# Kernel optimization log

Hardware: AMD Instinct MI355X
Metric: run time of the kernel (lower is better)

Reference implementation:

```python
import jax, jax.numpy as jnp
import numpy as np

EPS = 1e-7
B, C, IMG = 1024, 3, 32
NCLASS = 10
N_IN, L_IN, L_OUT = 64, 16, 16   # primary caps: 64 capsules of length 16; digit caps length 16
R_ITER = 3


def squash(c, axis):
    dot = jnp.sum(c * c, axis=axis, keepdims=True)
    return dot / (1.0 + dot) / jnp.sqrt(dot + EPS) * c


def conv2d(x, w, b, stride):
    y = jax.lax.conv_general_dilated(x, w, (stride, stride), 'VALID',
                                     dimension_numbers=('NCHW', 'OIHW', 'NCHW'))
    return y + b[None, :, None, None]


def setup_inputs() -> dict:
    key = jax.random.key(0)
    ks = jax.random.split(key, 16)
    inp = {
        'x': jax.random.uniform(ks[0], (B, C, IMG, IMG), dtype=jnp.float32),
        'y': jax.random.randint(ks[1], (B,), 0, NCLASS, dtype=jnp.int64),
        'conv1_w': 0.05 * jax.random.normal(ks[2], (128, C, 3, 3), jnp.float32),
        'conv1_b': jnp.zeros((128,), jnp.float32),
        'conv2_w': 0.05 * jax.random.normal(ks[3], (256, 128, 5, 5), jnp.float32),
        'conv2_b': jnp.zeros((256,), jnp.float32),
        'conv3_w': 0.05 * jax.random.normal(ks[4], (256, 256, 5, 5), jnp.float32),
        'conv3_b': jnp.zeros((256,), jnp.float32),
        'caps_w': 0.05 * jax.random.normal(ks[5], (N_IN, NCLASS, L_IN, L_OUT), jnp.float32),
        'caps_b': 0.05 * jax.random.normal(ks[6], (NCLASS, L_OUT), jnp.float32),
        'fc1_w': 0.05 * jax.random.normal(ks[7], (512, NCLASS * L_OUT), jnp.float32),
        'fc1_b': jnp.zeros((512,), jnp.float32),
        'fc2_w': 0.05 * jax.random.normal(ks[8], (1024, 512), jnp.float32),
        'fc2_b': jnp.zeros((1024,), jnp.float32),
        'fc3_w': 0.05 * jax.random.normal(ks[9], (IMG * IMG * C, 1024), jnp.float32),
        'fc3_b': jnp.zeros((IMG * IMG * C,), jnp.float32),
    }
    return inp


def reference(x, y, conv1_w, conv1_b, conv2_w, conv2_b, conv3_w, conv3_b,
              caps_w, caps_b, fc1_w, fc1_b, fc2_w, fc2_b, fc3_w, fc3_b):
    # CNN blocks
    h = jax.nn.relu(conv2d(x, conv1_w, conv1_b, 2))   # [B,128,15,15]
    h = jax.nn.relu(conv2d(h, conv2_w, conv2_b, 2))   # [B,256,6,6]
    h = jax.nn.relu(conv2d(h, conv3_w, conv3_b, 1))   # [B,256,2,2]

    # Primary capsules: [B,64,16], squashed along capsule-length axis
    prim = squash(h.reshape(h.shape[0], N_IN, L_IN), axis=-1)

    # u_hat[b,i,o,j] = sum_k W[i,o,k,j] * prim[b,i,k]  -> [B,64,10,16]
    u_hat = jnp.einsum('bik,iokj->bioj', prim, caps_w)
    u_hat_det = jax.lax.stop_gradient(u_hat)

    b_ij = jnp.zeros((h.shape[0], N_IN, NCLASS), dtype=u_hat.dtype)
    v = None
    for r in range(R_ITER):
        c_ij = jax.nn.softmax(b_ij, axis=2)           # over output capsules
        uh = u_hat if r == R_ITER - 1 else u_hat_det
        s = jnp.einsum('bio,bioj->boj', c_ij, uh) + caps_b   # [B,10,16]
        v = squash(s, axis=-1)
        if r < R_ITER - 1:
            agree = jnp.einsum('bioj,boj->bio', u_hat_det, jax.lax.stop_gradient(v))
            b_ij = b_ij + agree

    # capsule lengths: [B,10,1,1]
    v_lengths = jnp.sqrt(jnp.sum(v * v, axis=-1, keepdims=True) + EPS)[..., None]

    # reconstruction (mask by true label one-hot)
    one_hot = jax.nn.one_hot(y, NCLASS, dtype=v.dtype)       # [B,10]
    masked = (v * one_hot[:, :, None]).reshape(v.shape[0], NCLASS * L_OUT)
    h1 = jax.nn.relu(masked @ fc1_w.T + fc1_b)
    h2 = jax.nn.relu(h1 @ fc2_w.T + fc2_b)
    decoded = jax.nn.sigmoid(h2 @ fc3_w.T + fc3_b)           # [B,3072]
    return (v_lengths, decoded)
```

## Files before the change

kernel.cpp:

```cpp
#include <hip/hip_runtime.h>
#include <hip/hip_bf16.h>
#include <math.h>

#define EPSF 1e-7f

typedef __attribute__((ext_vector_type(8))) short bhalf8;
typedef __attribute__((ext_vector_type(4))) float floatx4;

__global__ __launch_bounds__(256) void conv1_kernel(
    const float* __restrict__ x, const float* __restrict__ w,
    const float* __restrict__ bias, __hip_bfloat16* __restrict__ out)
{
  __shared__ float wl[3456];
  __shared__ float bl[128];
  const int b = blockIdx.x;
  const int t = threadIdx.x;
  for (int i = t; i < 3456; i += 256) wl[i] = w[i];
  if (t < 128) bl[t] = bias[t];
  __syncthreads();
  if (t >= 225) return;
  const int py = t / 15, px = t % 15;
  const float* xb = x + b * 3072;
  float win[27];
#pragma unroll
  for (int c = 0; c < 3; ++c)
#pragma unroll
    for (int ky = 0; ky < 3; ++ky)
#pragma unroll
      for (int kx = 0; kx < 3; ++kx)
        win[c*9 + ky*3 + kx] = xb[c*1024 + (py*2 + ky)*32 + (px*2 + kx)];
#pragma unroll 1
  for (int oc0 = 0; oc0 < 128; oc0 += 32) {
    __hip_bfloat16 hv[32];
#pragma unroll
    for (int oc = 0; oc < 32; ++oc) {
      const float* wp = &wl[(oc0 + oc)*27];
      float acc = bl[oc0 + oc];
#pragma unroll
      for (int q = 0; q < 27; ++q) acc = fmaf(win[q], wp[q], acc);
      hv[oc] = __float2bfloat16(fmaxf(acc, 0.f));
    }
    uint4* dst = (uint4*)&out[((size_t)b*225 + t)*128 + oc0];
    const uint4* src = (const uint4*)hv;
#pragma unroll
    for (int q = 0; q < 4; ++q) dst[q] = src[q];
  }
}

__global__ __launch_bounds__(256) void prep_kernel(
    const float* __restrict__ conv2w, const float* __restrict__ conv3w,
    const float* __restrict__ capsw,  const float* __restrict__ fc1w,
    const float* __restrict__ fc2w,   const float* __restrict__ fc3w,
    __hip_bfloat16* __restrict__ wt2, __hip_bfloat16* __restrict__ wt3,
    __hip_bfloat16* __restrict__ cwt, float* __restrict__ fc1wt,
    __hip_bfloat16* __restrict__ wf2, __hip_bfloat16* __restrict__ wf3)
{
  const int t = threadIdx.x;
  int b = blockIdx.x;
  if (b < 12288) {
    int i = b*256 + t;
    wf3[i] = __float2bfloat16(fc3w[i]);
    return;
  }
  b -= 12288;
  if (b < 6400) {
    int i = b*256 + t;
    int s = i >> 14, r = i & 16383;
    int oc = r >> 6, kq = r & 63;
    int k = s*64 + kq;
    int tap = k >> 8, ic = k & 255;
    wt3[i] = __float2bfloat16(conv3w[(oc*256 + ic)*25 + tap]);
    return;
  }
  b -= 6400;
  if (b < 3200) {
    int i = b*256 + t;
    int s = i >> 13, r = i & 8191;
    int oc = r >> 5, kq = r & 31;
    int h = (s >= 50) ? 1 : 0;
    int r2 = s - h*50;
    int tap = r2 >> 1, q = r2 & 1;
    int ic = h*64 + q*32 + kq;
    wt2[i] = __float2bfloat16(conv2w[(oc*128 + ic)*25 + tap]);
    return;
  }
  b -= 3200;
  if (b < 2048) {
    int i = b*256 + t;
    wf2[i] = __float2bfloat16(fc2w[i]);
    return;
  }
  b -= 2048;
  if (b < 640) {
    int i2 = b*256 + t;
    int k = i2 & 15, j = (i2 >> 4) & 15, io = i2 >> 8;
    cwt[i2] = __float2bfloat16(capsw[(io*16 + k)*16 + j]);
    return;
  }
  b -= 640;
  {
    int i = b*256 + t;
    int j = i >> 9, n = i & 511;
    fc1wt[i] = fc1w[n*160 + j];
  }
}

__global__ __launch_bounds__(1024) void conv2_mfma_kernel(
    const __hip_bfloat16* __restrict__ a,
    const __hip_bfloat16* __restrict__ wt,
    const float* __restrict__ bias,
    __hip_bfloat16* __restrict__ out)
{
  __shared__ __align__(16) unsigned short Il[4*225*64];
  const int b0   = blockIdx.x * 4;
  const int t    = threadIdx.x;
  const int lane = t & 63;
  const int w    = t >> 6;
  const int wm   = w >> 3;
  const int wn   = w & 7;
  const int n    = lane & 15;
  const int g    = lane >> 4;

  const char* gB = (const char*)wt + (wn*32 + n)*64 + g*16;
  bhalf8 b00 = *(const bhalf8*)(gB);
  bhalf8 b01 = *(const bhalf8*)(gB + 1024);
  bhalf8 b10 = *(const bhalf8*)(gB + 16384);
  bhalf8 b11 = *(const bhalf8*)(gB + 16384 + 1024);

  int Abase[5], em[5];
#pragma unroll
  for (int mt = 0; mt < 5; ++mt) {
    int tile = wm*5 + mt;
    int m = tile*16 + n;
    if (m >= 144) m = 0;
    int img = m / 36, pos = m - img*36;
    int py = pos / 6, px = pos - py*6;
    int pixb = 30*py + 2*px;
    Abase[mt] = (img*225 + pixb) * 128;
    em[mt] = g + m;
  }

  floatx4 acc[5][2];
#pragma unroll
  for (int mt = 0; mt < 5; ++mt)
#pragma unroll
    for (int nt = 0; nt < 2; ++nt)
      acc[mt][nt] = (floatx4){0.f, 0.f, 0.f, 0.f};

  int s = 0;
#pragma unroll 1
  for (int h = 0; h < 2; ++h) {
    if (h) __syncthreads();
    for (int i = t; i < 7200; i += 1024) {
      int img = i / 1800;
      int r = i - img*1800;
      int p = r >> 3, c = r & 7;
      uint4 v = *(const uint4*)((const char*)a +
                ((size_t)(b0+img)*225 + p)*256 + h*128 + c*16);
      int px15 = p % 15, py15 = p / 15;
      int csw = (c + (px15 >> 1) + 6*(py15 >> 1) + ((img & 1) << 2)) & 7;
      *(uint4*)((char*)Il + (img*225 + p)*128 + csw*16) = v;
    }
    __syncthreads();

    int dpix = 0, kx = 0, ky = 0;
#pragma unroll 1
    for (int tap = 0; tap < 25; ++tap) {
      const int doff = dpix << 7;
      const int dsw  = (kx >> 1) + 6*(ky >> 1);
      int a0[5];
#pragma unroll
      for (int mt = 0; mt < 5; ++mt)
        a0[mt] = Abase[mt] + doff + (((em[mt] + dsw) & 7) << 4);

#pragma unroll
      for (int mt = 0; mt < 4; ++mt) {
        bhalf8 av = *(const bhalf8*)((const char*)Il + a0[mt]);
        acc[mt][0] = __builtin_amdgcn_mfma_f32_16x16x32_bf16(av, b00, acc[mt][0], 0, 0, 0);
        acc[mt][1] = __builtin_amdgcn_mfma_f32_16x16x32_bf16(av, b01, acc[mt][1], 0, 0, 0);
      }
      if (wm == 0) {
        bhalf8 av = *(const bhalf8*)((const char*)Il + a0[4]);
        acc[4][0] = __builtin_amdgcn_mfma_f32_16x16x32_bf16(av, b00, acc[4][0], 0, 0, 0);
        acc[4][1] = __builtin_amdgcn_mfma_f32_16x16x32_bf16(av, b01, acc[4][1], 0, 0, 0);
      }
      {
        const int spre = (s + 2 < 100) ? (s + 2) : 99;
        b00 = *(const bhalf8*)(gB + (size_t)spre*16384);
        b01 = *(const bhalf8*)(gB + (size_t)spre*16384 + 1024);
      }
#pragma unroll
      for (int mt = 0; mt < 4; ++mt) {
        bhalf8 av = *(const bhalf8*)((const char*)Il + (a0[mt] ^ 64));
        acc[mt][0] = __builtin_amdgcn_mfma_f32_16x16x32_bf16(av, b10, acc[mt][0], 0, 0, 0);
        acc[mt][1] = __builtin_amdgcn_mfma_f32_16x16x32_bf16(av, b11, acc[mt][1], 0, 0, 0);
      }
      if (wm == 0) {
        bhalf8 av = *(const bhalf8*)((const char*)Il + (a0[4] ^ 64));
        acc[4][0] = __builtin_amdgcn_mfma_f32_16x16x32_bf16(av, b10, acc[4][0], 0, 0, 0);
        acc[4][1] = __builtin_amdgcn_mfma_f32_16x16x32_bf16(av, b11, acc[4][1], 0, 0, 0);
      }
      {
        const int spre = (s + 3 < 100) ? (s + 3) : 99;
        b10 = *(const bhalf8*)(gB + (size_t)spre*16384);
        b11 = *(const bhalf8*)(gB + (size_t)spre*16384 + 1024);
      }
      s += 2;
      if (kx == 4) { kx = 0; ++ky; dpix += 11; } else { ++kx; ++dpix; }
    }
  }

  const float bv0 = bias[wn*32 + n];
  const float bv1 = bias[wn*32 + 16 + n];
#pragma unroll
  for (int mt = 0; mt < 5; ++mt) {
    if (mt < 4 || wm == 0) {
      int tile = wm*5 + mt;
#pragma unroll
      for (int r = 0; r < 4; ++r) {
        int m = tile*16 + g*4 + r;
        int img = m / 36, pos = m - img*36;
        size_t o = (((size_t)(b0+img)*36 + pos) << 8) + wn*32 + n;
        out[o]      = __float2bfloat16(fmaxf(acc[mt][0][r] + bv0, 0.f));
        out[o + 16] = __float2bfloat16(fmaxf(acc[mt][1][r] + bv1, 0.f));
      }
    }
  }
}

__global__ __launch_bounds__(512) void conv3_mfma_kernel(
    const __hip_bfloat16* __restrict__ a,
    const __hip_bfloat16* __restrict__ wt,
    float* __restrict__ pout)
{
  __shared__ __align__(16) unsigned short Il[16*1448];
  const int b0   = blockIdx.x * 16;
  const int kq   = blockIdx.y;
  const int t    = threadIdx.x;
  const int lane = t & 63;
  const int w    = t >> 6;
  const int n    = lane & 15;
  const int g    = lane >> 4;

  for (int i = t; i < 2304; i += 512) {
    int img = i / 144, r = i - img*144;
    int p = r >> 2, c = r & 3;
    uint4 v = *(const uint4*)((const char*)a +
              ((((size_t)(b0+img)*36 + p) << 9) + kq*64 + c*16));
    *(uint4*)((char*)Il + (img*1448 + p*40 + c*8)*2) = v;
  }

  const char* gB = (const char*)wt + (size_t)(w*32 + n)*128 +
                   (kq & 1)*64 + g*16;
  const int kqs = kq >> 1;
  bhalf8 b00, b01, b10, b11;
  b00 = *(const bhalf8*)(gB + (size_t)(0*4 + kqs)*32768);
  b01 = *(const bhalf8*)(gB + (size_t)(0*4 + kqs)*32768 + 2048);
  b10 = *(const bhalf8*)(gB + (size_t)(1*4 + kqs)*32768);
  b11 = *(const bhalf8*)(gB + (size_t)(1*4 + kqs)*32768 + 2048);

  const int d = n >> 2, pos = n & 3;
  const int pb = (pos >> 1)*6 + (pos & 1);
  int ab[4];
#pragma unroll
  for (int mt = 0; mt < 4; ++mt)
    ab[mt] = ((mt*4 + d)*1448 + pb*40 + g*8) * 2;

  floatx4 acc[4][2];
#pragma unroll
  for (int mt = 0; mt < 4; ++mt)
#pragma unroll
    for (int nt = 0; nt < 2; ++nt)
      acc[mt][nt] = (floatx4){0.f, 0.f, 0.f, 0.f};

  __syncthreads();

  int toff = 0, kx = 0;
#pragma unroll 1
  for (int tap = 0; tap < 24; tap += 2) {
#pragma unroll
    for (int mt = 0; mt < 4; ++mt) {
      bhalf8 av = *(const bhalf8*)((const char*)Il + ab[mt] + toff*80);
      acc[mt][0] = __builtin_amdgcn_mfma_f32_16x16x32_bf16(av, b00, acc[mt][0], 0, 0, 0);
      acc[mt][1] = __builtin_amdgcn_mfma_f32_16x16x32_bf16(av, b01, acc[mt][1], 0, 0, 0);
    }
    b00 = *(const bhalf8*)(gB + (size_t)((tap+2)*4 + kqs)*32768);
    b01 = *(const bhalf8*)(gB + (size_t)((tap+2)*4 + kqs)*32768 + 2048);
    if (++kx == 5) { kx = 0; toff += 2; } else ++toff;
#pragma unroll
    for (int mt = 0; mt < 4; ++mt) {
      bhalf8 av = *(const bhalf8*)((const char*)Il + ab[mt] + toff*80);
      acc[mt][0] = __builtin_amdgcn_mfma_f32_16x16x32_bf16(av, b10, acc[mt][0], 0, 0, 0);
      acc[mt][1] = __builtin_amdgcn_mfma_f32_16x16x32_bf16(av, b11, acc[mt][1], 0, 0, 0);
    }
    {
      const int tpre = (tap + 3 <= 24) ? (tap + 3) : 24;
      b10 = *(const bhalf8*)(gB + (size_t)(tpre*4 + kqs)*32768);
      b11 = *(const bhalf8*)(gB + (size_t)(tpre*4 + kqs)*32768 + 2048);
    }
    if (++kx == 5) { kx = 0; toff += 2; } else ++toff;
  }
#pragma unroll
  for (int mt = 0; mt < 4; ++mt) {
    bhalf8 av = *(const bhalf8*)((const char*)Il + ab[mt] + toff*80);
    acc[mt][0] = __builtin_amdgcn_mfma_f32_16x16x32_bf16(av, b00, acc[mt][0], 0, 0, 0);
    acc[mt][1] = __builtin_amdgcn_mfma_f32_16x16x32_bf16(av, b01, acc[mt][1], 0, 0, 0);
  }

  float* po = pout + (size_t)kq*1048576;
#pragma unroll
  for (int mt = 0; mt < 4; ++mt) {
#pragma unroll
    for (int r = 0; r < 4; ++r) {
      int m = mt*16 + g*4 + r;
      int img = m >> 2, p2 = m & 3;
#pragma unroll
      for (int nt = 0; nt < 2; ++nt)
        po[((size_t)(b0+img)*256 + w*32 + nt*16 + n)*4 + p2] = acc[mt][nt][r];
    }
  }
}

__global__ __launch_bounds__(256) void caps_kernel(
    const float* __restrict__ pout, const __hip_bfloat16* __restrict__ cwt,
    const float* __restrict__ cb, const float* __restrict__ c3b,
    const int* __restrict__ y,
    const float* __restrict__ fc1wt, const float* __restrict__ fc1b,
    float* __restrict__ vlen, __hip_bfloat16* __restrict__ h1f)
{
  __shared__ float prim[1024];
  __shared__ float uh[10240];
  __shared__ float bij[640];
  __shared__ float cij[640];
  __shared__ float vv[160];
  const int b = blockIdx.x, t = threadIdx.x;
  {
    const float* pp = pout + (size_t)b*1024 + t*4;
    float4 s4 = *(const float4*)pp;
#pragma unroll
    for (int q = 1; q < 8; ++q) {
      float4 v = *(const float4*)(pp + (size_t)q*1048576);
      s4.x += v.x; s4.y += v.y; s4.z += v.z; s4.w += v.w;
    }
    const float bv = c3b[t];
    float4 h = make_float4(fmaxf(s4.x + bv, 0.f), fmaxf(s4.y + bv, 0.f),
                           fmaxf(s4.z + bv, 0.f), fmaxf(s4.w + bv, 0.f));
    float dd = h.x*h.x + h.y*h.y + h.z*h.z + h.w*h.w;
    dd += __shfl_xor(dd, 1);
    dd += __shfl_xor(dd, 2);
    float sc = dd / (1.f + dd) / sqrtf(dd + EPSF);
    float4 o4 = make_float4(h.x*sc, h.y*sc, h.z*sc, h.w*sc);
    *(float4*)&prim[t*4] = o4;
  }
  for (int f = t; f < 640; f += 256) bij[f] = 0.f;
  __syncthreads();
  for (int f = t; f < 10240; f += 256) {
    const int i = f / 160;
    const uint4* wv = (const uint4*)(cwt + (size_t)f*16);
    uint4 wa = wv[0], wb = wv[1];
    unsigned uw[8] = {wa.x, wa.y, wa.z, wa.w, wb.x, wb.y, wb.z, wb.w};
    const float* pp = prim + i*16;
    float s = 0.f;
#pragma unroll
    for (int q = 0; q < 8; ++q) {
      float lo = __uint_as_float(uw[q] << 16);
      float hi = __uint_as_float(uw[q] & 0xffff0000u);
      s = fmaf(pp[2*q],   lo, s);
      s = fmaf(pp[2*q+1], hi, s);
    }
    uh[f] = s;
  }
  __syncthreads();
  for (int r = 0; r < 3; ++r) {
    if (t < 64) {
      float e[10];
      float mx = -1e30f;
#pragma unroll
      for (int o = 0; o < 10; ++o) { e[o] = bij[t*10 + o]; mx = fmaxf(mx, e[o]); }
      float sum = 0.f;
#pragma unroll
      for (int o = 0; o < 10; ++o) { e[o] = expf(e[o] - mx); sum += e[o]; }
      float inv = 1.f / sum;
#pragma unroll
      for (int o = 0; o < 10; ++o) cij[t*10 + o] = e[o] * inv;
    }
    __syncthreads();
    if (t < 160) {
      const int o = t >> 4;
      float s = cb[t];
      for (int i = 0; i < 64; ++i) s = fmaf(cij[i*10 + o], uh[i*160 + t], s);
      float dd = s*s;
      dd += __shfl_xor(dd, 1); dd += __shfl_xor(dd, 2);
      dd += __shfl_xor(dd, 4); dd += __shfl_xor(dd, 8);
      float sc = dd / (1.f + dd) / sqrtf(dd + EPSF);
      vv[t] = s * sc;
      if (r == 2 && (t & 15) == 0)
        vlen[b*10 + o] = sqrtf(sc*sc*dd + EPSF);
    }
    __syncthreads();
    if (r < 2) {
      for (int f = t; f < 640; f += 256) {
        int i = f / 10, o = f % 10;
        const float* up = &uh[i*160 + o*16];
        const float* vp = &vv[o*16];
        float a = 0.f;
#pragma unroll
        for (int j = 0; j < 16; ++j) a = fmaf(up[j], vp[j], a);
        bij[f] += a;
      }
      __syncthreads();
    }
  }
  const int yb = y[b];
  const float* vy = &vv[yb*16];
  for (int nn = t; nn < 512; nn += 256) {
    float s = fc1b[nn];
#pragma unroll
    for (int k = 0; k < 16; ++k)
      s = fmaf(vy[k], fc1wt[(yb*16 + k)*512 + nn], s);
    h1f[b*512 + nn] = __float2bfloat16(fmaxf(s, 0.f));
  }
}

template<int ACT, int MT, int NT>
__global__ __launch_bounds__(256) void fc_mfma_kernel(
    const __hip_bfloat16* __restrict__ A,
    const __hip_bfloat16* __restrict__ W,
    const float* __restrict__ bias,
    void* __restrict__ outv, int M, int N, int K)
{
  const int t    = threadIdx.x;
  const int lane = t & 63;
  const int w    = t >> 6;
  const int wr   = w >> 1, wc = w & 1;
  const int n    = lane & 15, g = lane >> 4;
  const int m0   = blockIdx.x * (2*MT*16) + wr*(MT*16);
  const int n0   = blockIdx.y * (2*NT*16) + wc*(NT*16);
  const __hip_bfloat16* Ap = A + (size_t)(m0 + n)*K + g*8;
  const __hip_bfloat16* Wp = W + (size_t)(n0 + n)*K + g*8;
  const int steps = K >> 5;

  bhalf8 aa0[MT], aa1[MT], bb0[NT], bb1[NT];
#pragma unroll
  for (int mt = 0; mt < MT; ++mt) {
    aa0[mt] = *(const bhalf8*)(Ap + (size_t)mt*16*K);
    aa1[mt] = *(const bhalf8*)(Ap + (size_t)mt*16*K + 32);
  }
#pragma unroll
  for (int nt = 0; nt < NT; ++nt) {
    bb0[nt] = *(const bhalf8*)(Wp + (size_t)nt*16*K);
    bb1[nt] = *(const bhalf8*)(Wp + (size_t)nt*16*K + 32);
  }

  floatx4 acc[MT][NT];
#pragma unroll
  for (int mt = 0; mt < MT; ++mt)
#pragma unroll
    for (int nt = 0; nt < NT; ++nt)
      acc[mt][nt] = (floatx4){0.f, 0.f, 0.f, 0.f};

#pragma unroll 1
  for (int s = 0; s < steps; s += 2) {
#pragma unroll
    for (int mt = 0; mt < MT; ++mt)
#pragma unroll
      for (int nt = 0; nt < NT; ++nt)
        acc[mt][nt] = __builtin_amdgcn_mfma_f32_16x16x32_bf16(
            aa0[mt], bb0[nt], acc[mt][nt], 0, 0, 0);
    {
      const int spre = (s + 2 < steps) ? (s + 2) : s;
#pragma unroll
      for (int mt = 0; mt < MT; ++mt)
        aa0[mt] = *(const bhalf8*)(Ap + (size_t)mt*16*K + spre*32);
#pragma unroll
      for (int nt = 0; nt < NT; ++nt)
        bb0[nt] = *(const bhalf8*)(Wp + (size_t)nt*16*K + spre*32);
    }
#pragma unroll
    for (int mt = 0; mt < MT; ++mt)
#pragma unroll
      for (int nt = 0; nt < NT; ++nt)
        acc[mt][nt] = __builtin_amdgcn_mfma_f32_16x16x32_bf16(
            aa1[mt], bb1[nt], acc[mt][nt], 0, 0, 0);
    {
      const int spre = (s + 3 < steps) ? (s + 3) : (s + 1);
#pragma unroll
      for (int mt = 0; mt < MT; ++mt)
        aa1[mt] = *(const bhalf8*)(Ap + (size_t)mt*16*K + spre*32);
#pragma unroll
      for (int nt = 0; nt < NT; ++nt)
        bb1[nt] = *(const bhalf8*)(Wp + (size_t)nt*16*K + spre*32);
    }
  }

#pragma unroll
  for (int mt = 0; mt < MT; ++mt) {
#pragma unroll
    for (int r = 0; r < 4; ++r) {
      const int m = m0 + mt*16 + g*4 + r;
#pragma unroll
      for (int nt = 0; nt < NT; ++nt) {
        const int col = n0 + nt*16 + n;
        float v = acc[mt][nt][r] + bias[col];
        if (ACT == 0) {
          ((__hip_bfloat16*)outv)[(size_t)m*N + col] =
              __float2bfloat16(fmaxf(v, 0.f));
        } else {
          ((float*)outv)[(size_t)m*N + col] = 1.f / (1.f + expf(-v));
        }
      }
    }
  }
}

extern "C" void kernel_launch(void* const* d_in, const int* in_sizes, int n_in,
                              void* d_out, int out_size, void* d_ws, size_t ws_size,
                              hipStream_t stream) {
  const float* x       = (const float*)d_in[0];
  const int*   y       = (const int*)  d_in[1];
  const float* conv1_w = (const float*)d_in[2];
  const float* conv1_b = (const float*)d_in[3];
  const float* conv2_w = (const float*)d_in[4];
  const float* conv2_b = (const float*)d_in[5];
  const float* conv3_w = (const float*)d_in[6];
  const float* conv3_b = (const float*)d_in[7];
  const float* caps_w  = (const float*)d_in[8];
  const float* caps_b  = (const float*)d_in[9];
  const float* fc1_w   = (const float*)d_in[10];
  const float* fc1_b   = (const float*)d_in[11];
  const float* fc2_w   = (const float*)d_in[12];
  const float* fc2_b   = (const float*)d_in[13];
  const float* fc3_w   = (const float*)d_in[14];
  const float* fc3_b   = (const float*)d_in[15];
  float* out = (float*)d_out;
  float* ws  = (float*)d_ws;

  __hip_bfloat16* h1t   = (__hip_bfloat16*)ws;
  __hip_bfloat16* wt2   = (__hip_bfloat16*)(ws + 14745600);
  __hip_bfloat16* wt3   = (__hip_bfloat16*)(ws + 15155200);
  __hip_bfloat16* h2t   = (__hip_bfloat16*)(ws + 15974400);
  float*          pout  = ws + 20692992;
  __hip_bfloat16* h1f   = (__hip_bfloat16*)(ws + 29081600);
  __hip_bfloat16* h2f   = (__hip_bfloat16*)(ws + 29343744);
  __hip_bfloat16* wf2   = (__hip_bfloat16*)(ws + 29868032);
  __hip_bfloat16* wf3   = (__hip_bfloat16*)(ws + 30130176);
  __hip_bfloat16* cwt   = (__hip_bfloat16*)(ws + 31703040);
  float*          fc1wt = ws + 31784960;

  prep_kernel<<<dim3(24896), 256, 0, stream>>>(
      conv2_w, conv3_w, caps_w, fc1_w, fc2_w, fc3_w,
      wt2, wt3, cwt, fc1wt, wf2, wf3);
  conv1_kernel<<<dim3(1024),       256, 0, stream>>>(x, conv1_w, conv1_b, h1t);
  conv2_mfma_kernel<<<dim3(256),  1024, 0, stream>>>(h1t, wt2, conv2_b, h2t);
  conv3_mfma_kernel<<<dim3(64, 8), 512, 0, stream>>>(h2t, wt3, pout);
  caps_kernel<<<dim3(1024),        256, 0, stream>>>(pout, cwt, caps_b, conv3_b,
                                                     y, fc1wt, fc1_b, out, h1f);
  fc_mfma_kernel<0,2,2><<<dim3(16, 16), 256, 0, stream>>>(
      h1f, wf2, fc2_b, h2f, 1024, 1024, 512);
  fc_mfma_kernel<1,2,2><<<dim3(16, 48), 256, 0, stream>>>(
      h2f, wf3, fc3_b, out + 10240, 1024, 3072, 1024);
}
```

Baseline: 340.4 us.

## Process two images per conv1 block and store conv1 output channel-chunk-major

conv1 now computes two images per block, padding the per-channel weights to 32 floats so they can be read as float4 and sharing each weight load across both images. Its bf16 output changes from pixel-major (225x128) to 16-channel-chunk-major, so each 16-byte store from adjacent threads lands contiguously. conv2's staging load is updated to read that layout. The caps routing sum is split into four independent accumulators to shorten the FMA dependency chain, which slightly changes the summation order.

```diff
diff --git a/kernel.cpp b/kernel.cpp
--- a/kernel.cpp
+++ b/kernel.cpp
@@ -11,39 +11,58 @@
     const float* __restrict__ x, const float* __restrict__ w,
     const float* __restrict__ bias, __hip_bfloat16* __restrict__ out)
 {
-  __shared__ float wl[3456];
+  __shared__ float wl[4096];
   __shared__ float bl[128];
-  const int b = blockIdx.x;
+  const int b0 = blockIdx.x * 2;
   const int t = threadIdx.x;
-  for (int i = t; i < 3456; i += 256) wl[i] = w[i];
+  for (int i = t; i < 4096; i += 256) {
+    int oc = i >> 5, q = i & 31;
+    wl[i] = (q < 27) ? w[oc*27 + q] : 0.f;
+  }
   if (t < 128) bl[t] = bias[t];
   __syncthreads();
   if (t >= 225) return;
   const int py = t / 15, px = t % 15;
-  const float* xb = x + b * 3072;
-  float win[27];
-#pragma unroll
-  for (int c = 0; c < 3; ++c)
-#pragma unroll
-    for (int ky = 0; ky < 3; ++ky)
-#pragma unroll
-      for (int kx = 0; kx < 3; ++kx)
-        win[c*9 + ky*3 + kx] = xb[c*1024 + (py*2 + ky)*32 + (px*2 + kx)];
+  float win[2][28];
+  win[0][27] = 0.f; win[1][27] = 0.f;
+#pragma unroll
+  for (int im = 0; im < 2; ++im) {
+    const float* xb = x + (size_t)(b0 + im) * 3072;
+#pragma unroll
+    for (int c = 0; c < 3; ++c)
+#pragma unroll
+      for (int ky = 0; ky < 3; ++ky)
+#pragma unroll
+        for (int kx = 0; kx < 3; ++kx)
+          win[im][c*9 + ky*3 + kx] = xb[c*1024 + (py*2 + ky)*32 + (px*2 + kx)];
+  }
 #pragma unroll 1
   for (int oc0 = 0; oc0 < 128; oc0 += 32) {
-    __hip_bfloat16 hv[32];
+    __hip_bfloat16 hv[2][32];
 #pragma unroll
     for (int oc = 0; oc < 32; ++oc) {
-      const float* wp = &wl[(oc0 + oc)*27];
-      float acc = bl[oc0 + oc];
-#pragma unroll
-      for (int q = 0; q < 27; ++q) acc = fmaf(win[q], wp[q], acc);
-      hv[oc] = __float2bfloat16(fmaxf(acc, 0.f));
-    }
-    uint4* dst = (uint4*)&out[((size_t)b*225 + t)*128 + oc0];
-    const uint4* src = (const uint4*)hv;
-#pragma unroll
-    for (int q = 0; q < 4; ++q) dst[q] = src[q];
+      const float4* wp = (const float4*)&wl[(oc0 + oc) << 5];
+      float a0 = bl[oc0 + oc], a1 = a0;
+#pragma unroll
+      for (int qq = 0; qq < 7; ++qq) {
+        float4 wv = wp[qq];
+        a0 = fmaf(win[0][qq*4+0], wv.x, a0); a1 = fmaf(win[1][qq*4+0], wv.x, a1);
+        a0 = fmaf(win[0][qq*4+1], wv.y, a0); a1 = fmaf(win[1][qq*4+1], wv.y, a1);
+        a0 = fmaf(win[0][qq*4+2], wv.z, a0); a1 = fmaf(win[1][qq*4+2], wv.z, a1);
+        a0 = fmaf(win[0][qq*4+3], wv.w, a0); a1 = fmaf(win[1][qq*4+3], wv.w, a1);
+      }
+      hv[0][oc] = __float2bfloat16(fmaxf(a0, 0.f));
+      hv[1][oc] = __float2bfloat16(fmaxf(a1, 0.f));
+    }
+#pragma unroll
+    for (int qq = 0; qq < 4; ++qq) {
+      int c16 = (oc0 >> 3) + qq;
+#pragma unroll
+      for (int im = 0; im < 2; ++im) {
+        const uint4* src = (const uint4*)hv[im];
+        *(uint4*)((char*)out + (size_t)(b0+im)*57600 + c16*3600 + t*16) = src[qq];
+      }
+    }
   }
 }
 
@@ -105,14 +124,15 @@
   }
 }
 
-__global__ __launch_bounds__(1024) void conv2_mfma_kernel(
+__global__ __launch_bounds__(1024) void conv2_mfma_v2_kernel(
     const __hip_bfloat16* __restrict__ a,
     const __hip_bfloat16* __restrict__ wt,
     const float* __restrict__ bias,
-    __hip_bfloat16* __restrict__ out)
+    __hip_bfloat16* __restrict__ out,
+    int img_base)
 {
   __shared__ __align__(16) unsigned short Il[4*225*64];
-  const int b0   = blockIdx.x * 4;
+  const int b0   = img_base + blockIdx.x * 4;
   const int t    = threadIdx.x;
   const int lane = t & 63;
   const int w    = t >> 6;
@@ -156,7 +176,7 @@
       int r = i - img*1800;
       int p = r >> 3, c = r & 7;
       uint4 v = *(const uint4*)((const char*)a +
-                ((size_t)(b0+img)*225 + p)*256 + h*128 + c*16);
+                (size_t)(b0+img)*57600 + (h*8 + c)*3600 + p*16);
       int px15 = p % 15, py15 = p / 15;
       int csw = (c + (px15 >> 1) + 6*(py15 >> 1) + ((img & 1) << 2)) & 7;
       *(uint4*)((char*)Il + (img*225 + p)*128 + csw*16) = v;
@@ -387,8 +407,14 @@
     __syncthreads();
     if (t < 160) {
       const int o = t >> 4;
-      float s = cb[t];
-      for (int i = 0; i < 64; ++i) s = fmaf(cij[i*10 + o], uh[i*160 + t], s);
+      float s0 = cb[t], s1 = 0.f, s2 = 0.f, s3 = 0.f;
+      for (int i = 0; i < 64; i += 4) {
+        s0 = fmaf(cij[(i+0)*10 + o], uh[(i+0)*160 + t], s0);
+        s1 = fmaf(cij[(i+1)*10 + o], uh[(i+1)*160 + t], s1);
+        s2 = fmaf(cij[(i+2)*10 + o], uh[(i+2)*160 + t], s2);
+        s3 = fmaf(cij[(i+3)*10 + o], uh[(i+3)*160 + t], s3);
+      }
+      float s = (s0 + s1) + (s2 + s3);
       float dd = s*s;
       dd += __shfl_xor(dd, 1); dd += __shfl_xor(dd, 2);
       dd += __shfl_xor(dd, 4); dd += __shfl_xor(dd, 8);
@@ -550,8 +576,8 @@
   prep_kernel<<<dim3(24896), 256, 0, stream>>>(
       conv2_w, conv3_w, caps_w, fc1_w, fc2_w, fc3_w,
       wt2, wt3, cwt, fc1wt, wf2, wf3);
-  conv1_kernel<<<dim3(1024),       256, 0, stream>>>(x, conv1_w, conv1_b, h1t);
-  conv2_mfma_kernel<<<dim3(256),  1024, 0, stream>>>(h1t, wt2, conv2_b, h2t);
+  conv1_kernel<<<dim3(512),        256, 0, stream>>>(x, conv1_w, conv1_b, h1t);
+  conv2_mfma_v2_kernel<<<dim3(256), 1024, 0, stream>>>(h1t, wt2, conv2_b, h2t, 0);
   conv3_mfma_kernel<<<dim3(64, 8), 512, 0, stream>>>(h2t, wt3, pout);
   caps_kernel<<<dim3(1024),        256, 0, stream>>>(pout, cwt, caps_b, conv3_b,
                                                      y, fc1wt, fc1_b, out, h1f);
```

Result: no change. 340.0 us (-0.1%).
